# Optimization experiments

Measured on AMD Instinct MI355X. Metric: run time of the kernel, lower is better.

Reference implementation:

```python
import jax, jax.numpy as jnp
import numpy as np

B = 2048          # batch_size
D = 512           # embedding dim
TEMP = 0.1        # temperature
EPS = 1e-8        # torch CosineSimilarity eps


def _neg_idx(batch_size):
    n = 2 * batch_size
    mask = np.eye(n) + np.eye(n, n, k=-batch_size) + np.eye(n, n, k=batch_size)
    mask = (1 - mask).astype(bool)           # True at negatives
    # each row has exactly n-2 True entries -> fixed-shape gather indices
    return np.nonzero(mask)[1].reshape(n, n - 2)

_NEG_IDX = jnp.asarray(_neg_idx(B))           # [2B, 2B-2]
_ROWS = jnp.arange(2 * B)[:, None]            # [2B, 1]


def _cos_sim_matrix(r):
    # r: [2B, D] -> [2B, 2B] cosine similarity
    norm = jnp.maximum(jnp.linalg.norm(r, axis=-1, keepdims=True), EPS)
    rn = r / norm
    return rn @ rn.T


def _pos(sim):
    # diag(sim, +B) and diag(sim, -B), concatenated -> [2B, 1]
    l = jnp.diagonal(sim, offset=B)
    r = jnp.diagonal(sim, offset=-B)
    return jnp.concatenate([l, r])[:, None]


def _neg(sim):
    # masked gather of off-(diag,+B,-B) entries -> [2B, 2B-2]
    return sim[_ROWS, _NEG_IDX]


def _ce_sum_label0(logits):
    # CrossEntropyLoss(reduction='sum') with all labels == 0
    return -jnp.sum(jax.nn.log_softmax(logits, axis=-1)[:, 0])


def setup_inputs() -> dict:
    key = jax.random.key(0)
    k1, k2, k3, k4 = jax.random.split(key, 4)
    return {
        "z_ori": jax.random.normal(k1, (B, D), jnp.float32),
        "z_hard_pos": jax.random.normal(k2, (B, D), jnp.float32),
        "z_soft_pos": jax.random.normal(k3, (B, D), jnp.float32),
        "z_soft_neg": jax.random.normal(k4, (B, D), jnp.float32),
    }


def reference(z_ori, z_hard_pos, z_soft_pos, z_soft_neg):
    sim_ori_hp = _cos_sim_matrix(jnp.concatenate([z_ori, z_hard_pos], axis=0))
    sim_ori_sp = _cos_sim_matrix(jnp.concatenate([z_ori, z_soft_pos], axis=0))
    sim_ori_sn = _cos_sim_matrix(jnp.concatenate([z_ori, z_soft_neg], axis=0))
    sim_hp_sp = _cos_sim_matrix(jnp.concatenate([z_hard_pos, z_soft_pos], axis=0))
    sim_hp_sn = _cos_sim_matrix(jnp.concatenate([z_hard_pos, z_soft_neg], axis=0))
    sim_sp_sn = _cos_sim_matrix(jnp.concatenate([z_soft_pos, z_soft_neg], axis=0))

    pos_ori_sn = _pos(sim_ori_sn)
    pos_hp_sn = _pos(sim_hp_sn)
    pos_sp_sn = _pos(sim_sp_sn)

    pos_ori_hp = _pos(sim_ori_hp)
    neg_ori_hp = _neg(sim_ori_hp)
    pos_ori_sp = _pos(sim_ori_sp)
    neg_ori_sp = _neg(sim_ori_sp)
    pos_hp_sp = _pos(sim_hp_sp)
    neg_hp_sp = _neg(sim_hp_sp)

    logits_ori_hp = jnp.concatenate([pos_ori_hp, neg_ori_hp, pos_ori_sn], axis=1) / TEMP
    logits_ori_sp = jnp.concatenate([pos_ori_sp, neg_ori_sp, pos_ori_sn], axis=1) / TEMP
    logits_hp_sp = jnp.concatenate([pos_hp_sp, neg_hp_sp, pos_hp_sn, pos_sp_sn], axis=1) / TEMP

    denom = 2.0 * B
    return (
        _ce_sum_label0(logits_ori_hp) / denom,
        _ce_sum_label0(logits_ori_sp) / denom,
        _ce_sum_label0(logits_hp_sp) / denom,
    )
```

## Files before the change

kernel.cpp:

```cpp
#include <hip/hip_runtime.h>
#include <hip/hip_bf16.h>

#define Bn 2048
#define Dn 512

typedef float f32x4 __attribute__((ext_vector_type(4)));
typedef long long ll2 __attribute__((ext_vector_type(2)));

typedef __attribute__((address_space(1))) const unsigned int gas_u32;
typedef __attribute__((address_space(3))) unsigned int las_u32;

__device__ __forceinline__ void gload16(const void* g, void* l) {
  __builtin_amdgcn_global_load_lds((gas_u32*)g, (las_u32*)l, 16, 0, 0);
}

__global__ __launch_bounds__(256) void normalize_kernel(
    const float* __restrict__ in0, const float* __restrict__ in1,
    const float* __restrict__ in2, const float* __restrict__ in3,
    unsigned char* __restrict__ nm8, float* __restrict__ rs, float* __restrict__ dd) {
  __shared__ float sv[4][Dn];
  __shared__ float red[4][6];
  int row = blockIdx.x;
  int wave = threadIdx.x >> 6, lane = threadIdx.x & 63;

  int g0 = blockIdx.x * 256 + threadIdx.x;
  if (g0 < 9 * Bn) rs[g0] = 0.0f;

  const float* src =
      (wave == 0 ? in0 : wave == 1 ? in1 : wave == 2 ? in2 : in3) + (size_t)row * Dn;
  int k = lane * 8;
  float4 x0 = *(const float4*)(src + k);
  float4 x1 = *(const float4*)(src + k + 4);
  float v[8] = {x0.x, x0.y, x0.z, x0.w, x1.x, x1.y, x1.z, x1.w};
  float ss = 0.f;
#pragma unroll
  for (int e = 0; e < 8; e++) ss = fmaf(v[e], v[e], ss);
#pragma unroll
  for (int off = 1; off < 64; off <<= 1) ss += __shfl_xor(ss, off, 64);
  float scale = 1.0f / fmaxf(sqrtf(ss), 1e-8f);
  float nv[8];
#pragma unroll
  for (int e = 0; e < 8; e++) {
    nv[e] = v[e] * scale;
    sv[wave][k + e] = nv[e];
  }
  if (wave < 3) {
    unsigned int lo = __builtin_amdgcn_cvt_pk_fp8_f32(nv[0], nv[1], 0u, false);
    lo = __builtin_amdgcn_cvt_pk_fp8_f32(nv[2], nv[3], lo, true);
    unsigned int hi = __builtin_amdgcn_cvt_pk_fp8_f32(nv[4], nv[5], 0u, false);
    hi = __builtin_amdgcn_cvt_pk_fp8_f32(nv[6], nv[7], hi, true);
    uint2 pk; pk.x = lo; pk.y = hi;
    int kb = lane >> 3, g = lane & 7;
    int p = ((g & 3) << 1) | (g >> 2);
    *(uint2*)(nm8 + ((size_t)wave * Bn + row) * Dn + kb * 64 + p * 8) = pk;
  }
  __syncthreads();

  int t = threadIdx.x;
  float o0 = sv[0][2 * t], o1 = sv[0][2 * t + 1];
  float h0 = sv[1][2 * t], h1 = sv[1][2 * t + 1];
  float p0 = sv[2][2 * t], p1 = sv[2][2 * t + 1];
  float n0 = sv[3][2 * t], n1 = sv[3][2 * t + 1];
  float s[6];
  s[0] = fmaf(o0, h0, o1 * h1);
  s[1] = fmaf(o0, p0, o1 * p1);
  s[2] = fmaf(h0, p0, h1 * p1);
  s[3] = fmaf(o0, n0, o1 * n1);
  s[4] = fmaf(h0, n0, h1 * n1);
  s[5] = fmaf(p0, n0, p1 * n1);
#pragma unroll
  for (int off = 1; off < 64; off <<= 1) {
#pragma unroll
    for (int j = 0; j < 6; j++) s[j] += __shfl_xor(s[j], off, 64);
  }
  if (lane == 0) {
#pragma unroll
    for (int j = 0; j < 6; j++) red[wave][j] = s[j];
  }
  __syncthreads();
  if (threadIdx.x < 6) {
    int j = threadIdx.x;
    dd[j * Bn + row] = red[0][j] + red[1][j] + red[2][j] + red[3][j];
  }
}

#define GBM 128
#define NKT 8

__global__ __launch_bounds__(512, 4) void gemm_fp8_kernel(const unsigned char* __restrict__ nm8,
                                                          float* __restrict__ rs) {
  __shared__ unsigned char As[65536];
  __shared__ float cb[2 * GBM];

  int id = ((int)blockIdx.x & 7) * 147 + ((int)blockIdx.x >> 3);
  int by = 0, rem = id, cnt = 48;
  while (rem >= cnt) { rem -= cnt; by++; cnt--; }
  int bx = by + rem;
  int u = by >> 4, v = bx >> 4;
  int rrow, rcol;
  if (u == v) { rrow = u; rcol = u; }
  else if (u == 0) { if (v == 1) { rrow = 3; rcol = 4; } else { rrow = 5; rcol = 6; } }
  else { rrow = 7; rcol = 8; }

  const unsigned char* gA = nm8 + ((size_t)u * Bn + (size_t)(by & 15) * GBM) * Dn;
  const unsigned char* gB = nm8 + ((size_t)v * Bn + (size_t)(bx & 15) * GBM) * Dn;

  int tid = threadIdx.x, lane = tid & 63, wave = tid >> 6;
  int wr = wave >> 2, wc = wave & 3;
  int c = lane & 15, rgrp = lane >> 4;

  {
    int usrc = (tid & 31) ^ ((tid >> 5) & 15);
    const unsigned char* sA = gA + (size_t)(tid >> 5) * Dn + usrc * 16;
    char* dA = (char*)As + (wave << 10);
#pragma unroll
    for (int j = 0; j < 8; ++j) gload16(sA + j * 8192, dA + j * 8192);
  }

  const unsigned char* pb0 = gB + (size_t)(wc * 32 + c) * Dn + rgrp * 16;
  const unsigned char* pb1 = pb0 + (size_t)16 * Dn;
  ll2 b[3][2];
#pragma unroll
  for (int t = 0; t < 3; ++t) {
    b[t][0] = *(const ll2*)(pb0 + t * 64);
    b[t][1] = *(const ll2*)(pb1 + t * 64);
  }

  __syncthreads();

  int abase = (wr * 64 + c) * 512;

  f32x4 acc[4][2] = {};
#pragma unroll
  for (int t = 0; t < NKT; ++t) {
    int uoff = (((t * 4 + rgrp) ^ c) << 4);
    ll2 a[4];
#pragma unroll
    for (int mi = 0; mi < 4; ++mi)
      a[mi] = *(const ll2*)(As + abase + mi * 8192 + uoff);
    if (t + 3 < NKT) {
      b[(t + 3) % 3][0] = *(const ll2*)(pb0 + (t + 3) * 64);
      b[(t + 3) % 3][1] = *(const ll2*)(pb1 + (t + 3) * 64);
    }
    __builtin_amdgcn_s_setprio(1);
#pragma unroll
    for (int ks = 0; ks < 2; ++ks)
#pragma unroll
      for (int mi = 0; mi < 4; ++mi)
#pragma unroll
        for (int ni = 0; ni < 2; ++ni)
          acc[mi][ni] = __builtin_amdgcn_mfma_f32_16x16x32_fp8_fp8(
              a[mi][ks], b[t % 3][ni][ks], acc[mi][ni], 0, 0, 0);
    __builtin_amdgcn_s_setprio(0);
  }

  if (tid < 2 * GBM) cb[tid] = 0.0f;
  __syncthreads();
  float* crow = cb;
  float* ccol = cb + GBM;

  bool skip_diag = (by == bx);
#pragma unroll
  for (int mi = 0; mi < 4; ++mi)
#pragma unroll
    for (int ni = 0; ni < 2; ++ni)
#pragma unroll
      for (int r = 0; r < 4; ++r) {
        int lrow = wr * 64 + mi * 16 + rgrp * 4 + r;
        int lcol = wc * 32 + ni * 16 + c;
        float e = __expf(10.0f * acc[mi][ni][r] - 10.0f);
        acc[mi][ni][r] = (skip_diag && lrow == lcol) ? 0.0f : e;
      }

#pragma unroll
  for (int mi = 0; mi < 4; ++mi)
#pragma unroll
    for (int r = 0; r < 4; ++r) {
      float val = acc[mi][0][r] + acc[mi][1][r];
      val += __shfl_xor(val, 1, 64);
      val += __shfl_xor(val, 2, 64);
      val += __shfl_xor(val, 4, 64);
      val += __shfl_xor(val, 8, 64);
      if (c == 0) atomicAdd(&crow[wr * 64 + mi * 16 + rgrp * 4 + r], val);
    }
#pragma unroll
  for (int ni = 0; ni < 2; ++ni) {
    float cv = 0.f;
#pragma unroll
    for (int mi = 0; mi < 4; ++mi)
#pragma unroll
      for (int r = 0; r < 4; ++r) cv += acc[mi][ni][r];
    cv += __shfl_xor(cv, 16, 64);
    cv += __shfl_xor(cv, 32, 64);
    if (lane < 16) atomicAdd(&ccol[wc * 32 + ni * 16 + c], cv);
  }
  __syncthreads();

  float* rs_row = rs + rrow * Bn + (by & 15) * GBM;
  if (tid < GBM) {
    atomicAdd(rs_row + tid, crow[tid]);
  } else if (tid < 2 * GBM && by != bx) {
    float* rs_col = rs + rcol * Bn + (bx & 15) * GBM;
    atomicAdd(rs_col + (tid - GBM), ccol[tid - GBM]);
  }
}

__global__ __launch_bounds__(1024) void final_kernel(const float* __restrict__ rs,
                                                     const float* __restrict__ dd,
                                                     float* __restrict__ out) {
  int tid = threadIdx.x;
  float l1 = 0.f, l2 = 0.f, l3 = 0.f;
  for (int i = tid; i < Bn; i += 1024) {
    float doh = dd[i], dop = dd[Bn + i], dhp = dd[2 * Bn + i];
    float ea = __expf(10.0f * dd[3 * Bn + i] - 10.0f);
    float eb = __expf(10.0f * dd[4 * Bn + i] - 10.0f);
    float ec = __expf(10.0f * dd[5 * Bn + i] - 10.0f);
    float r0 = rs[i], r1 = rs[Bn + i], r2 = rs[2 * Bn + i];
    float r3 = rs[3 * Bn + i], r4 = rs[4 * Bn + i], r5 = rs[5 * Bn + i];
    float r6 = rs[6 * Bn + i], r7 = rs[7 * Bn + i], r8 = rs[8 * Bn + i];
    l1 += 20.0f + logf(r0 + r3 + ea) + logf(r4 + r1 + ea) - 20.0f * doh;
    l2 += 20.0f + logf(r0 + r5 + ea) + logf(r6 + r2 + ea) - 20.0f * dop;
    l3 += 20.0f + logf(r1 + r7 + eb + ec) + logf(r8 + r2 + eb + ec) - 20.0f * dhp;
  }
  __shared__ float red[3][1024];
  red[0][tid] = l1; red[1][tid] = l2; red[2][tid] = l3;
  __syncthreads();
  for (int s = 512; s > 0; s >>= 1) {
    if (tid < s) {
      red[0][tid] += red[0][tid + s];
      red[1][tid] += red[1][tid + s];
      red[2][tid] += red[2][tid + s];
    }
    __syncthreads();
  }
  if (tid == 0) {
    out[0] = red[0][0] / 4096.0f;
    out[1] = red[1][0] / 4096.0f;
    out[2] = red[2][0] / 4096.0f;
  }
}

extern "C" void kernel_launch(void* const* d_in, const int* in_sizes, int n_in,
                              void* d_out, int out_size, void* d_ws, size_t ws_size,
                              hipStream_t stream) {
  const float* z0 = (const float*)d_in[0];
  const float* z1 = (const float*)d_in[1];
  const float* z2 = (const float*)d_in[2];
  const float* z3 = (const float*)d_in[3];
  float* out = (float*)d_out;

  unsigned char* nm8 = (unsigned char*)d_ws;
  float* rs = (float*)((char*)d_ws + (size_t)3 * Bn * Dn);
  float* dd = rs + 9 * Bn;

  hipLaunchKernelGGL(normalize_kernel, dim3(2048), dim3(256), 0, stream,
                     z0, z1, z2, z3, nm8, rs, dd);
  hipLaunchKernelGGL(gemm_fp8_kernel, dim3(1176), dim3(512), 0, stream, nm8, rs);
  hipLaunchKernelGGL(final_kernel, dim3(1), dim3(1024), 0, stream, rs, dd, out);
}
```

Baseline: 47.32 us.

## Switch FP8 GEMM to 16x16x128 scaled MFMA with natural K layout

```diff
diff --git a/kernel.cpp b/kernel.cpp
--- a/kernel.cpp
+++ b/kernel.cpp
@@ -5,7 +5,9 @@
 #define Dn 512
 
 typedef float f32x4 __attribute__((ext_vector_type(4)));
-typedef long long ll2 __attribute__((ext_vector_type(2)));
+typedef int v8i __attribute__((ext_vector_type(8)));
+
+union V8 { int4 q[2]; v8i v; };
 
 typedef __attribute__((address_space(1))) const unsigned int gas_u32;
 typedef __attribute__((address_space(3))) unsigned int las_u32;
@@ -50,9 +52,7 @@
     unsigned int hi = __builtin_amdgcn_cvt_pk_fp8_f32(nv[4], nv[5], 0u, false);
     hi = __builtin_amdgcn_cvt_pk_fp8_f32(nv[6], nv[7], hi, true);
     uint2 pk; pk.x = lo; pk.y = hi;
-    int kb = lane >> 3, g = lane & 7;
-    int p = ((g & 3) << 1) | (g >> 2);
-    *(uint2*)(nm8 + ((size_t)wave * Bn + row) * Dn + kb * 64 + p * 8) = pk;
+    *(uint2*)(nm8 + ((size_t)wave * Bn + row) * Dn + k) = pk;
   }
   __syncthreads();
 
@@ -85,10 +85,10 @@
 }
 
 #define GBM 128
-#define NKT 8
-
-__global__ __launch_bounds__(512, 4) void gemm_fp8_kernel(const unsigned char* __restrict__ nm8,
-                                                          float* __restrict__ rs) {
+#define NKT 4
+
+__global__ __launch_bounds__(512) void gemm_fp8_kernel(const unsigned char* __restrict__ nm8,
+                                                       float* __restrict__ rs) {
   __shared__ unsigned char As[65536];
   __shared__ float cb[2 * GBM];
 
@@ -108,49 +108,56 @@
   int tid = threadIdx.x, lane = tid & 63, wave = tid >> 6;
   int wr = wave >> 2, wc = wave & 3;
   int c = lane & 15, rgrp = lane >> 4;
+  int cx = c & 7;
 
   {
-    int usrc = (tid & 31) ^ ((tid >> 5) & 15);
+    int usrc = (tid & 31) ^ ((tid >> 5) & 7);
     const unsigned char* sA = gA + (size_t)(tid >> 5) * Dn + usrc * 16;
     char* dA = (char*)As + (wave << 10);
 #pragma unroll
     for (int j = 0; j < 8; ++j) gload16(sA + j * 8192, dA + j * 8192);
   }
 
-  const unsigned char* pb0 = gB + (size_t)(wc * 32 + c) * Dn + rgrp * 16;
+  const unsigned char* pb0 = gB + (size_t)(wc * 32 + c) * Dn + rgrp * 32;
   const unsigned char* pb1 = pb0 + (size_t)16 * Dn;
-  ll2 b[3][2];
-#pragma unroll
-  for (int t = 0; t < 3; ++t) {
-    b[t][0] = *(const ll2*)(pb0 + t * 64);
-    b[t][1] = *(const ll2*)(pb1 + t * 64);
+  V8 b[3][2];
+#pragma unroll
+  for (int t = 0; t < 2; ++t) {
+    b[t][0].q[0] = *(const int4*)(pb0 + t * 128);
+    b[t][0].q[1] = *(const int4*)(pb0 + t * 128 + 16);
+    b[t][1].q[0] = *(const int4*)(pb1 + t * 128);
+    b[t][1].q[1] = *(const int4*)(pb1 + t * 128 + 16);
   }
 
   __syncthreads();
 
   int abase = (wr * 64 + c) * 512;
-
   f32x4 acc[4][2] = {};
 #pragma unroll
   for (int t = 0; t < NKT; ++t) {
-    int uoff = (((t * 4 + rgrp) ^ c) << 4);
-    ll2 a[4];
+    int u0 = ((t * 8 + rgrp * 2) ^ cx) * 16;
+    int u1 = ((t * 8 + rgrp * 2 + 1) ^ cx) * 16;
+    V8 a[4];
+#pragma unroll
+    for (int mi = 0; mi < 4; ++mi) {
+      a[mi].q[0] = *(const int4*)(As + abase + mi * 8192 + u0);
+      a[mi].q[1] = *(const int4*)(As + abase + mi * 8192 + u1);
+    }
+    if (t + 2 < NKT) {
+      int sl = (t + 2) % 3;
+      b[sl][0].q[0] = *(const int4*)(pb0 + (t + 2) * 128);
+      b[sl][0].q[1] = *(const int4*)(pb0 + (t + 2) * 128 + 16);
+      b[sl][1].q[0] = *(const int4*)(pb1 + (t + 2) * 128);
+      b[sl][1].q[1] = *(const int4*)(pb1 + (t + 2) * 128 + 16);
+    }
+    __builtin_amdgcn_s_setprio(1);
 #pragma unroll
     for (int mi = 0; mi < 4; ++mi)
-      a[mi] = *(const ll2*)(As + abase + mi * 8192 + uoff);
-    if (t + 3 < NKT) {
-      b[(t + 3) % 3][0] = *(const ll2*)(pb0 + (t + 3) * 64);
-      b[(t + 3) % 3][1] = *(const ll2*)(pb1 + (t + 3) * 64);
-    }
-    __builtin_amdgcn_s_setprio(1);
-#pragma unroll
-    for (int ks = 0; ks < 2; ++ks)
-#pragma unroll
-      for (int mi = 0; mi < 4; ++mi)
-#pragma unroll
-        for (int ni = 0; ni < 2; ++ni)
-          acc[mi][ni] = __builtin_amdgcn_mfma_f32_16x16x32_fp8_fp8(
-              a[mi][ks], b[t % 3][ni][ks], acc[mi][ni], 0, 0, 0);
+#pragma unroll
+      for (int ni = 0; ni < 2; ++ni)
+        acc[mi][ni] = __builtin_amdgcn_mfma_scale_f32_16x16x128_f8f6f4(
+            a[mi].v, b[t % 3][ni].v, acc[mi][ni], 0, 0,
+            0, 0x7F7F7F7F, 0, 0x7F7F7F7F);
     __builtin_amdgcn_s_setprio(0);
   }
 
```

New measurement: 62.76 us. 32.6% more time.

## Process two column tiles per block reusing the LDS-resident A tile

Applied to the files above, without the earlier changes.

```diff
diff --git a/kernel.cpp b/kernel.cpp
--- a/kernel.cpp
+++ b/kernel.cpp
@@ -87,23 +87,90 @@
 #define GBM 128
 #define NKT 8
 
+#define KLOOP(PB0, PB1)                                                      \
+  _Pragma("unroll") for (int t = 0; t < NKT; ++t) {                          \
+    int uoff = (((t * 4 + rgrp) ^ c) << 4);                                  \
+    ll2 a[4];                                                                \
+    _Pragma("unroll") for (int mi = 0; mi < 4; ++mi)                         \
+        a[mi] = *(const ll2*)(As + abase + mi * 8192 + uoff);                \
+    if (t + 2 < NKT) {                                                       \
+      int sl = (t + 2) % 3;                                                  \
+      b[sl][0] = *(const ll2*)((PB0) + (t + 2) * 64);                        \
+      b[sl][1] = *(const ll2*)((PB1) + (t + 2) * 64);                        \
+    }                                                                        \
+    __builtin_amdgcn_s_setprio(1);                                           \
+    _Pragma("unroll") for (int ks = 0; ks < 2; ++ks)                         \
+        _Pragma("unroll") for (int mi = 0; mi < 4; ++mi)                     \
+            _Pragma("unroll") for (int ni = 0; ni < 2; ++ni)                 \
+                acc[mi][ni] = __builtin_amdgcn_mfma_f32_16x16x32_fp8_fp8(    \
+                    a[mi][ks], b[t % 3][ni][ks], acc[mi][ni], 0, 0, 0);      \
+    __builtin_amdgcn_s_setprio(0);                                           \
+  }
+
+#define EPILOGUE(BY, BX)                                                     \
+  {                                                                          \
+    __syncthreads();                                                         \
+    if (tid < 2 * GBM) cb[tid] = 0.0f;                                       \
+    __syncthreads();                                                         \
+    bool skip_diag = ((BY) == (BX));                                         \
+    _Pragma("unroll") for (int mi = 0; mi < 4; ++mi)                         \
+        _Pragma("unroll") for (int ni = 0; ni < 2; ++ni)                     \
+            _Pragma("unroll") for (int r = 0; r < 4; ++r) {                  \
+      int lrow = wr * 64 + mi * 16 + rgrp * 4 + r;                           \
+      int lcol = wc * 32 + ni * 16 + c;                                      \
+      float e = __expf(10.0f * acc[mi][ni][r] - 10.0f);                      \
+      acc[mi][ni][r] = (skip_diag && lrow == lcol) ? 0.0f : e;               \
+    }                                                                        \
+    _Pragma("unroll") for (int mi = 0; mi < 4; ++mi)                         \
+        _Pragma("unroll") for (int r = 0; r < 4; ++r) {                      \
+      float val = acc[mi][0][r] + acc[mi][1][r];                             \
+      val += __shfl_xor(val, 1, 64);                                         \
+      val += __shfl_xor(val, 2, 64);                                         \
+      val += __shfl_xor(val, 4, 64);                                         \
+      val += __shfl_xor(val, 8, 64);                                         \
+      if (c == 0) atomicAdd(&cb[wr * 64 + mi * 16 + rgrp * 4 + r], val);     \
+    }                                                                        \
+    _Pragma("unroll") for (int ni = 0; ni < 2; ++ni) {                       \
+      float cv = 0.f;                                                        \
+      _Pragma("unroll") for (int mi = 0; mi < 4; ++mi)                       \
+          _Pragma("unroll") for (int r = 0; r < 4; ++r) cv += acc[mi][ni][r];\
+      cv += __shfl_xor(cv, 16, 64);                                          \
+      cv += __shfl_xor(cv, 32, 64);                                          \
+      if (lane < 16) atomicAdd(&cb[GBM + wc * 32 + ni * 16 + c], cv);        \
+    }                                                                        \
+    __syncthreads();                                                         \
+    int u2 = (BY) >> 4, v2 = (BX) >> 4;                                      \
+    int rrow, rcol;                                                          \
+    if (u2 == v2) { rrow = u2; rcol = u2; }                                  \
+    else if (u2 == 0) {                                                      \
+      if (v2 == 1) { rrow = 3; rcol = 4; } else { rrow = 5; rcol = 6; }      \
+    } else { rrow = 7; rcol = 8; }                                           \
+    if (tid < GBM) {                                                         \
+      atomicAdd(rs + rrow * Bn + ((BY) & 15) * GBM + tid, cb[tid]);          \
+    } else if (tid < 2 * GBM && (BY) != (BX)) {                              \
+      atomicAdd(rs + rcol * Bn + ((BX) & 15) * GBM + (tid - GBM),            \
+                cb[tid]);                                                    \
+    }                                                                        \
+  }
+
 __global__ __launch_bounds__(512, 4) void gemm_fp8_kernel(const unsigned char* __restrict__ nm8,
                                                           float* __restrict__ rs) {
   __shared__ unsigned char As[65536];
   __shared__ float cb[2 * GBM];
 
-  int id = ((int)blockIdx.x & 7) * 147 + ((int)blockIdx.x >> 3);
-  int by = 0, rem = id, cnt = 48;
-  while (rem >= cnt) { rem -= cnt; by++; cnt--; }
-  int bx = by + rem;
-  int u = by >> 4, v = bx >> 4;
-  int rrow, rcol;
-  if (u == v) { rrow = u; rcol = u; }
-  else if (u == 0) { if (v == 1) { rrow = 3; rcol = 4; } else { rrow = 5; rcol = 6; } }
-  else { rrow = 7; rcol = 8; }
-
-  const unsigned char* gA = nm8 + ((size_t)u * Bn + (size_t)(by & 15) * GBM) * Dn;
-  const unsigned char* gB = nm8 + ((size_t)v * Bn + (size_t)(bx & 15) * GBM) * Dn;
+  int id = ((int)blockIdx.x & 7) * 75 + ((int)blockIdx.x >> 3);
+  int by = 0, rem = id;
+  while (true) {
+    int np = (49 - by) >> 1;
+    if (rem < np) break;
+    rem -= np;
+    ++by;
+  }
+  int bx0 = by + 2 * rem;
+  bool has2 = (bx0 + 1 < 48);
+
+  const unsigned char* gA =
+      nm8 + ((size_t)(by >> 4) * Bn + (size_t)(by & 15) * GBM) * Dn;
 
   int tid = threadIdx.x, lane = tid & 63, wave = tid >> 6;
   int wr = wave >> 2, wc = wave & 3;
@@ -117,91 +184,45 @@
     for (int j = 0; j < 8; ++j) gload16(sA + j * 8192, dA + j * 8192);
   }
 
-  const unsigned char* pb0 = gB + (size_t)(wc * 32 + c) * Dn + rgrp * 16;
+  const unsigned char* gB1 =
+      nm8 + ((size_t)(bx0 >> 4) * Bn + (size_t)(bx0 & 15) * GBM) * Dn;
+  const unsigned char* pb0 = gB1 + (size_t)(wc * 32 + c) * Dn + rgrp * 16;
   const unsigned char* pb1 = pb0 + (size_t)16 * Dn;
   ll2 b[3][2];
-#pragma unroll
-  for (int t = 0; t < 3; ++t) {
-    b[t][0] = *(const ll2*)(pb0 + t * 64);
-    b[t][1] = *(const ll2*)(pb1 + t * 64);
-  }
+  b[0][0] = *(const ll2*)(pb0);
+  b[0][1] = *(const ll2*)(pb1);
+  b[1][0] = *(const ll2*)(pb0 + 64);
+  b[1][1] = *(const ll2*)(pb1 + 64);
 
   __syncthreads();
 
   int abase = (wr * 64 + c) * 512;
-
   f32x4 acc[4][2] = {};
-#pragma unroll
-  for (int t = 0; t < NKT; ++t) {
-    int uoff = (((t * 4 + rgrp) ^ c) << 4);
-    ll2 a[4];
+
+  KLOOP(pb0, pb1)
+
+  int bx1 = bx0 + 1;
+  const unsigned char* gB2 =
+      nm8 + ((size_t)(bx1 >> 4) * Bn + (size_t)((bx1 & 15) & 15) * GBM) * Dn;
+  const unsigned char* qb0 = gB2 + (size_t)(wc * 32 + c) * Dn + rgrp * 16;
+  const unsigned char* qb1 = qb0 + (size_t)16 * Dn;
+  if (has2) {
+    b[0][0] = *(const ll2*)(qb0);
+    b[0][1] = *(const ll2*)(qb1);
+    b[1][0] = *(const ll2*)(qb0 + 64);
+    b[1][1] = *(const ll2*)(qb1 + 64);
+  }
+
+  EPILOGUE(by, bx0)
+
+  if (has2) {
 #pragma unroll
     for (int mi = 0; mi < 4; ++mi)
-      a[mi] = *(const ll2*)(As + abase + mi * 8192 + uoff);
-    if (t + 3 < NKT) {
-      b[(t + 3) % 3][0] = *(const ll2*)(pb0 + (t + 3) * 64);
-      b[(t + 3) % 3][1] = *(const ll2*)(pb1 + (t + 3) * 64);
-    }
-    __builtin_amdgcn_s_setprio(1);
-#pragma unroll
-    for (int ks = 0; ks < 2; ++ks)
-#pragma unroll
-      for (int mi = 0; mi < 4; ++mi)
-#pragma unroll
-        for (int ni = 0; ni < 2; ++ni)
-          acc[mi][ni] = __builtin_amdgcn_mfma_f32_16x16x32_fp8_fp8(
-              a[mi][ks], b[t % 3][ni][ks], acc[mi][ni], 0, 0, 0);
-    __builtin_amdgcn_s_setprio(0);
-  }
-
-  if (tid < 2 * GBM) cb[tid] = 0.0f;
-  __syncthreads();
-  float* crow = cb;
-  float* ccol = cb + GBM;
-
-  bool skip_diag = (by == bx);
-#pragma unroll
-  for (int mi = 0; mi < 4; ++mi)
-#pragma unroll
-    for (int ni = 0; ni < 2; ++ni)
-#pragma unroll
-      for (int r = 0; r < 4; ++r) {
-        int lrow = wr * 64 + mi * 16 + rgrp * 4 + r;
-        int lcol = wc * 32 + ni * 16 + c;
-        float e = __expf(10.0f * acc[mi][ni][r] - 10.0f);
-        acc[mi][ni][r] = (skip_diag && lrow == lcol) ? 0.0f : e;
-      }
-
-#pragma unroll
-  for (int mi = 0; mi < 4; ++mi)
-#pragma unroll
-    for (int r = 0; r < 4; ++r) {
-      float val = acc[mi][0][r] + acc[mi][1][r];
-      val += __shfl_xor(val, 1, 64);
-      val += __shfl_xor(val, 2, 64);
-      val += __shfl_xor(val, 4, 64);
-      val += __shfl_xor(val, 8, 64);
-      if (c == 0) atomicAdd(&crow[wr * 64 + mi * 16 + rgrp * 4 + r], val);
-    }
-#pragma unroll
-  for (int ni = 0; ni < 2; ++ni) {
-    float cv = 0.f;
-#pragma unroll
-    for (int mi = 0; mi < 4; ++mi)
-#pragma unroll
-      for (int r = 0; r < 4; ++r) cv += acc[mi][ni][r];
-    cv += __shfl_xor(cv, 16, 64);
-    cv += __shfl_xor(cv, 32, 64);
-    if (lane < 16) atomicAdd(&ccol[wc * 32 + ni * 16 + c], cv);
-  }
-  __syncthreads();
-
-  float* rs_row = rs + rrow * Bn + (by & 15) * GBM;
-  if (tid < GBM) {
-    atomicAdd(rs_row + tid, crow[tid]);
-  } else if (tid < 2 * GBM && by != bx) {
-    float* rs_col = rs + rcol * Bn + (bx & 15) * GBM;
-    atomicAdd(rs_col + (tid - GBM), ccol[tid - GBM]);
+#pragma unroll
+      for (int ni = 0; ni < 2; ++ni) acc[mi][ni] = (f32x4){0.f, 0.f, 0.f, 0.f};
+
+    KLOOP(qb0, qb1)
+    EPILOGUE(by, bx1)
   }
 }
 
@@ -255,6 +276,6 @@
 
   hipLaunchKernelGGL(normalize_kernel, dim3(2048), dim3(256), 0, stream,
                      z0, z1, z2, z3, nm8, rs, dd);
-  hipLaunchKernelGGL(gemm_fp8_kernel, dim3(1176), dim3(512), 0, stream, nm8, rs);
+  hipLaunchKernelGGL(gemm_fp8_kernel, dim3(600), dim3(512), 0, stream, nm8, rs);
   hipLaunchKernelGGL(final_kernel, dim3(1), dim3(1024), 0, stream, rs, dd, out);
 }
```

Measured after the change: 52.58 us. 1.11x slower.
